# Optimization experiments

Measured on AMD Instinct MI355X. Metric: run time of the kernel, lower is better.

The kernel has to match this reference:

```python
import jax, jax.numpy as jnp
import numpy as np

LEAK = 0.01   # torch LeakyReLU default negative_slope
EPS = 1e-5    # torch BatchNorm2d default eps


def setup_inputs() -> dict:
    key = jax.random.key(0)
    ks = jax.random.split(key, 7)
    x = jax.random.normal(ks[0], (1, 64, 512, 512), jnp.float32)
    W = jax.random.normal(ks[1], (128, 64, 3, 3), jnp.float32) * 0.05
    gamma = jax.random.uniform(ks[2], (128,), jnp.float32, 0.5, 1.5)
    beta = jax.random.normal(ks[3], (128,), jnp.float32) * 0.1
    mean = jax.random.normal(ks[4], (128,), jnp.float32) * 0.1
    var = jax.random.uniform(ks[5], (128,), jnp.float32, 0.5, 1.5)
    # random.choices(rate=[0,1,1,...,1]) -> Bernoulli(0.9) mask over (1,C,H*W)
    mask = jax.random.bernoulli(ks[6], 0.9, (1, 128, 512, 512)).astype(jnp.int32)
    return dict(x=x, W=W, gamma=gamma, beta=beta, mean=mean, var=var, mask=mask)


def reference(x, W, gamma, beta, mean, var, mask):
    # 3x3 conv, stride 1, reflect padding 1, no bias
    xp = jnp.pad(x, ((0, 0), (0, 0), (1, 1), (1, 1)), mode='reflect')
    y = jax.lax.conv_general_dilated(
        xp, W, window_strides=(1, 1), padding='VALID',
        dimension_numbers=('NCHW', 'OIHW', 'NCHW'))
    # BatchNorm2d (inference mode: running stats)
    inv = jax.lax.rsqrt(var + EPS)
    scale = (gamma * inv)[None, :, None, None]
    shift = (beta - mean * gamma * inv)[None, :, None, None]
    y = y * scale + shift
    # Dropout2d(0.3) is identity in eval; LeakyReLU
    y = jnp.where(y >= 0, y, LEAK * y)
    # host-generated Bernoulli(0.9) mask multiply (the reshape to (1,C,1,H*W)
    # and back is a no-op on the math)
    return y * mask.astype(y.dtype)
```

## Files before the change

kernel.cpp:

```cpp
#include <hip/hip_runtime.h>

typedef unsigned short u16;
typedef unsigned int u32;
typedef __bf16 bf16x8 __attribute__((ext_vector_type(8)));
typedef float floatx4 __attribute__((ext_vector_type(4)));

#define EPS   1e-5f
#define LEAK  0.01f

#define TILE_H 4
#define TILE_W 64
#define IN_H   6
#define IN_W   66
#define CPAD   72

#define XT_BYTES ((size_t)512 * 512 * 64 * 2)
#define WT_BYTES ((size_t)9 * 128 * 64 * 2)

__device__ __forceinline__ u16 f2bf(float f) {
    union { float f; u32 i; } v; v.f = f;
    u32 i = v.i;
    return (u16)((i + 0x7fffu + ((i >> 16) & 1u)) >> 16);
}
__device__ __forceinline__ bf16x8 ld_frag(const u16* p) {
    uint4 d = *(const uint4*)p;
    return __builtin_bit_cast(bf16x8, d);
}

__global__ __launch_bounds__(256) void transpose_x(const float* __restrict__ x,
                                                   u16* __restrict__ xt)
{
    __shared__ u32 t[64][65];
    const int tid = threadIdx.x;
    const int s0  = blockIdx.x << 6;

    #pragma unroll
    for (int it = 0; it < 4; ++it) {
        int idx = it * 256 + tid;
        int ci = idx >> 4, wq = idx & 15;
        float4 d = *(const float4*)(x + (ci << 18) + s0 + (wq << 2));
        u32* row = &t[ci][wq << 2];
        row[0] = f2bf(d.x); row[1] = f2bf(d.y);
        row[2] = f2bf(d.z); row[3] = f2bf(d.w);
    }
    __syncthreads();
    #pragma unroll
    for (int it = 0; it < 2; ++it) {
        int idx = it * 256 + tid;
        int sl = idx >> 3, cb = idx & 7;
        uint4 o;
        o.x = t[cb * 8 + 0][sl] | (t[cb * 8 + 1][sl] << 16);
        o.y = t[cb * 8 + 2][sl] | (t[cb * 8 + 3][sl] << 16);
        o.z = t[cb * 8 + 4][sl] | (t[cb * 8 + 5][sl] << 16);
        o.w = t[cb * 8 + 6][sl] | (t[cb * 8 + 7][sl] << 16);
        *(uint4*)(xt + ((s0 + sl) << 6) + (cb << 3)) = o;
    }
}

__global__ __launch_bounds__(256) void transpose_w(const float* __restrict__ w,
                                                   u16* __restrict__ wt)
{
    int idx = blockIdx.x * 256 + threadIdx.x;
    int r   = idx >> 13;
    int rem = idx & 8191;
    wt[idx] = f2bf(w[rem * 9 + r]);
}

__global__ __launch_bounds__(256) void conv_mfma(
    const u16* __restrict__ xt,   const u16* __restrict__ wt,
    const float* __restrict__ gamma, const float* __restrict__ beta,
    const float* __restrict__ mean,  const float* __restrict__ var,
    const int* __restrict__ mask, float* __restrict__ out)
{
    __shared__ float s_scale[128];
    __shared__ float s_shift[128];
    __shared__ __attribute__((aligned(16))) u16 s_tile[IN_H * IN_W * CPAD];

    const int tid = threadIdx.x;
    const int bid = blockIdx.x;
    const int oh0 = (bid >> 3) << 2;
    const int ow0 = (bid & 7) << 6;

    if (tid < 128) {
        float sc = gamma[tid] * rsqrtf(var[tid] + EPS);
        s_scale[tid] = sc;
        s_shift[tid] = beta[tid] - mean[tid] * sc;
    }

    #pragma unroll
    for (int it = 0; it < 13; ++it) {
        int idx = it * 256 + tid;
        if (idx < IN_H * IN_W * 8) {
            int pos = idx >> 3, cb = idx & 7;
            int ihl = pos / IN_W;
            int iwl = pos - ihl * IN_W;
            int sh = oh0 - 1 + ihl; sh = sh < 0 ? -sh : (sh > 511 ? 1022 - sh : sh);
            int sw = ow0 - 1 + iwl; sw = sw < 0 ? -sw : (sw > 511 ? 1022 - sw : sw);
            uint4 d = *(const uint4*)(xt + (((sh << 9) + sw) << 6) + (cb << 3));
            *(uint4*)(s_tile + (ihl * IN_W + iwl) * CPAD + (cb << 3)) = d;
        }
    }
    __syncthreads();

    const int wave = tid >> 6;
    const int lane = tid & 63;
    const int quad = lane >> 4;
    const int l16  = lane & 15;
    const int mi   = wave >> 1;
    const int ni   = wave & 1;

    floatx4 acc[4][8];
    #pragma unroll
    for (int i = 0; i < 4; ++i)
        #pragma unroll
        for (int j = 0; j < 8; ++j)
            acc[i][j] = (floatx4){0.f, 0.f, 0.f, 0.f};

    int bbase[8];
    #pragma unroll
    for (int ns = 0; ns < 8; ++ns) {
        int n = ni * 128 + ns * 16 + l16;
        bbase[ns] = ((n >> 6) * IN_W + (n & 63)) * CPAD + quad * 8;
    }
    const u16* wbase = wt + (mi << 12) + (l16 << 6) + quad * 8;

    bf16x8 af_next[4];
    #pragma unroll
    for (int cs = 0; cs < 4; ++cs)
        af_next[cs] = ld_frag(wbase + (cs << 10));

    #pragma unroll 1
    for (int kc = 0; kc < 18; ++kc) {
        const int r    = kc >> 1;
        const int kh   = r / 3;
        const int kw   = r - kh * 3;
        const int cib  = (kc & 1) << 5;
        const int boff = (kh * IN_W + kw) * CPAD + cib;

        bf16x8 af[4];
        #pragma unroll
        for (int cs = 0; cs < 4; ++cs) af[cs] = af_next[cs];

        if (kc < 17) {
            const int kc1  = kc + 1;
            const int r1   = kc1 >> 1;
            const int cib1 = (kc1 & 1) << 5;
            #pragma unroll
            for (int cs = 0; cs < 4; ++cs)
                af_next[cs] = ld_frag(wbase + r1 * 8192 + (cs << 10) + cib1);
        }

        bf16x8 bfr[8];
        #pragma unroll
        for (int ns = 0; ns < 8; ++ns)
            bfr[ns] = ld_frag(s_tile + bbase[ns] + boff);

        #pragma unroll
        for (int cs = 0; cs < 4; ++cs)
            #pragma unroll
            for (int ns = 0; ns < 8; ++ns)
                acc[cs][ns] = __builtin_amdgcn_mfma_f32_16x16x32_bf16(
                    af[cs], bfr[ns], acc[cs][ns], 0, 0, 0);
    }

    int nbase[8];
    #pragma unroll
    for (int ns = 0; ns < 8; ++ns) {
        int n = ni * 128 + ns * 16 + l16;
        nbase[ns] = ((oh0 + (n >> 6)) << 9) + ow0 + (n & 63);
    }
    #pragma unroll
    for (int cs = 0; cs < 4; ++cs) {
        const int co0 = mi * 64 + cs * 16 + quad * 4;
        #pragma unroll
        for (int reg = 0; reg < 4; ++reg) {
            const int co = co0 + reg;
            const float sc = s_scale[co], sh = s_shift[co];
            const int cbase = co << 18;
            #pragma unroll
            for (int ns = 0; ns < 8; ++ns) {
                int idx = cbase + nbase[ns];
                float y = acc[cs][ns][reg] * sc + sh;
                y = (y >= 0.f) ? y : LEAK * y;
                y = mask[idx] ? y : 0.f;
                __builtin_nontemporal_store(y, &out[idx]);
            }
        }
    }
}

extern "C" void kernel_launch(void* const* d_in, const int* in_sizes, int n_in,
                              void* d_out, int out_size, void* d_ws, size_t ws_size,
                              hipStream_t stream)
{
    (void)in_sizes; (void)n_in; (void)out_size; (void)ws_size;
    const float* x     = (const float*)d_in[0];
    const float* W     = (const float*)d_in[1];
    const float* gamma = (const float*)d_in[2];
    const float* beta  = (const float*)d_in[3];
    const float* mean  = (const float*)d_in[4];
    const float* var   = (const float*)d_in[5];
    const int*   mask  = (const int*)d_in[6];
    float* out = (float*)d_out;

    u16* xt = (u16*)d_ws;
    u16* wt = (u16*)((char*)d_ws + XT_BYTES);

    transpose_w<<<288, 256, 0, stream>>>(W, wt);
    transpose_x<<<4096, 256, 0, stream>>>(x, xt);
    conv_mfma<<<1024, 256, 0, stream>>>(xt, wt, gamma, beta, mean, var, mask, out);
}
```

Baseline: 360.2 us.

## Fuse input transpose into conv kernel and shrink tile for occupancy

Drops the separate x-to-bf16 NHWC transpose kernel and its workspace round-trip. The conv kernel now reads fp32 NCHW input directly and converts to bf16 while staging into LDS. The output tile is halved to 4x32, giving 2048 blocks with fewer accumulators and a launch-bounds occupancy hint of 3. Mask loads become nontemporal. In exchange, the global loads during staging are strided by channel and less coalesced, and the larger halo ratio adds redundant input reads.

```diff
diff --git a/kernel.cpp b/kernel.cpp
--- a/kernel.cpp
+++ b/kernel.cpp
@@ -8,14 +8,10 @@
 #define EPS   1e-5f
 #define LEAK  0.01f
 
-#define TILE_H 4
-#define TILE_W 64
 #define IN_H   6
-#define IN_W   66
+#define IN_W   34
+#define NPOS   (IN_H * IN_W)
 #define CPAD   72
-
-#define XT_BYTES ((size_t)512 * 512 * 64 * 2)
-#define WT_BYTES ((size_t)9 * 128 * 64 * 2)
 
 __device__ __forceinline__ u16 f2bf(float f) {
     union { float f; u32 i; } v; v.f = f;
@@ -27,36 +23,6 @@
     return __builtin_bit_cast(bf16x8, d);
 }
 
-__global__ __launch_bounds__(256) void transpose_x(const float* __restrict__ x,
-                                                   u16* __restrict__ xt)
-{
-    __shared__ u32 t[64][65];
-    const int tid = threadIdx.x;
-    const int s0  = blockIdx.x << 6;
-
-    #pragma unroll
-    for (int it = 0; it < 4; ++it) {
-        int idx = it * 256 + tid;
-        int ci = idx >> 4, wq = idx & 15;
-        float4 d = *(const float4*)(x + (ci << 18) + s0 + (wq << 2));
-        u32* row = &t[ci][wq << 2];
-        row[0] = f2bf(d.x); row[1] = f2bf(d.y);
-        row[2] = f2bf(d.z); row[3] = f2bf(d.w);
-    }
-    __syncthreads();
-    #pragma unroll
-    for (int it = 0; it < 2; ++it) {
-        int idx = it * 256 + tid;
-        int sl = idx >> 3, cb = idx & 7;
-        uint4 o;
-        o.x = t[cb * 8 + 0][sl] | (t[cb * 8 + 1][sl] << 16);
-        o.y = t[cb * 8 + 2][sl] | (t[cb * 8 + 3][sl] << 16);
-        o.z = t[cb * 8 + 4][sl] | (t[cb * 8 + 5][sl] << 16);
-        o.w = t[cb * 8 + 6][sl] | (t[cb * 8 + 7][sl] << 16);
-        *(uint4*)(xt + ((s0 + sl) << 6) + (cb << 3)) = o;
-    }
-}
-
 __global__ __launch_bounds__(256) void transpose_w(const float* __restrict__ w,
                                                    u16* __restrict__ wt)
 {
@@ -66,20 +32,20 @@
     wt[idx] = f2bf(w[rem * 9 + r]);
 }
 
-__global__ __launch_bounds__(256) void conv_mfma(
-    const u16* __restrict__ xt,   const u16* __restrict__ wt,
+__global__ __launch_bounds__(256, 3) void conv_mfma(
+    const float* __restrict__ x,  const u16* __restrict__ wt,
     const float* __restrict__ gamma, const float* __restrict__ beta,
     const float* __restrict__ mean,  const float* __restrict__ var,
     const int* __restrict__ mask, float* __restrict__ out)
 {
     __shared__ float s_scale[128];
     __shared__ float s_shift[128];
-    __shared__ __attribute__((aligned(16))) u16 s_tile[IN_H * IN_W * CPAD];
+    __shared__ __attribute__((aligned(16))) u16 s_tile[NPOS * CPAD];
 
     const int tid = threadIdx.x;
     const int bid = blockIdx.x;
-    const int oh0 = (bid >> 3) << 2;
-    const int ow0 = (bid & 7) << 6;
+    const int oh0 = (bid >> 4) << 2;
+    const int ow0 = (bid & 15) << 5;
 
     if (tid < 128) {
         float sc = gamma[tid] * rsqrtf(var[tid] + EPS);
@@ -88,16 +54,25 @@
     }
 
     #pragma unroll
-    for (int it = 0; it < 13; ++it) {
-        int idx = it * 256 + tid;
-        if (idx < IN_H * IN_W * 8) {
-            int pos = idx >> 3, cb = idx & 7;
+    for (int it = 0; it < 7; ++it) {
+        int i = it * 256 + tid;
+        if (i < NPOS * 8) {
+            int cb  = i / NPOS;
+            int pos = i - cb * NPOS;
             int ihl = pos / IN_W;
             int iwl = pos - ihl * IN_W;
             int sh = oh0 - 1 + ihl; sh = sh < 0 ? -sh : (sh > 511 ? 1022 - sh : sh);
             int sw = ow0 - 1 + iwl; sw = sw < 0 ? -sw : (sw > 511 ? 1022 - sw : sw);
-            uint4 d = *(const uint4*)(xt + (((sh << 9) + sw) << 6) + (cb << 3));
-            *(uint4*)(s_tile + (ihl * IN_W + iwl) * CPAD + (cb << 3)) = d;
+            const float* src = x + (((size_t)cb << 21)) + (sh << 9) + sw;
+            float v0 = src[0 << 18], v1 = src[1 << 18], v2 = src[2 << 18],
+                  v3 = src[3 << 18], v4 = src[4 << 18], v5 = src[5 << 18],
+                  v6 = src[6 << 18], v7 = src[7 << 18];
+            uint4 p;
+            p.x = (u32)f2bf(v0) | ((u32)f2bf(v1) << 16);
+            p.y = (u32)f2bf(v2) | ((u32)f2bf(v3) << 16);
+            p.z = (u32)f2bf(v4) | ((u32)f2bf(v5) << 16);
+            p.w = (u32)f2bf(v6) | ((u32)f2bf(v7) << 16);
+            *(uint4*)(s_tile + pos * CPAD + (cb << 3)) = p;
         }
     }
     __syncthreads();
@@ -109,18 +84,18 @@
     const int mi   = wave >> 1;
     const int ni   = wave & 1;
 
-    floatx4 acc[4][8];
+    floatx4 acc[4][4];
     #pragma unroll
     for (int i = 0; i < 4; ++i)
         #pragma unroll
-        for (int j = 0; j < 8; ++j)
+        for (int j = 0; j < 4; ++j)
             acc[i][j] = (floatx4){0.f, 0.f, 0.f, 0.f};
 
-    int bbase[8];
+    int bbase[4];
     #pragma unroll
-    for (int ns = 0; ns < 8; ++ns) {
-        int n = ni * 128 + ns * 16 + l16;
-        bbase[ns] = ((n >> 6) * IN_W + (n & 63)) * CPAD + quad * 8;
+    for (int ns = 0; ns < 4; ++ns) {
+        int n = ni * 64 + ns * 16 + l16;
+        bbase[ns] = ((n >> 5) * IN_W + (n & 31)) * CPAD + quad * 8;
     }
     const u16* wbase = wt + (mi << 12) + (l16 << 6) + quad * 8;
 
@@ -150,24 +125,24 @@
                 af_next[cs] = ld_frag(wbase + r1 * 8192 + (cs << 10) + cib1);
         }
 
-        bf16x8 bfr[8];
+        bf16x8 bfr[4];
         #pragma unroll
-        for (int ns = 0; ns < 8; ++ns)
+        for (int ns = 0; ns < 4; ++ns)
             bfr[ns] = ld_frag(s_tile + bbase[ns] + boff);
 
         #pragma unroll
         for (int cs = 0; cs < 4; ++cs)
             #pragma unroll
-            for (int ns = 0; ns < 8; ++ns)
+            for (int ns = 0; ns < 4; ++ns)
                 acc[cs][ns] = __builtin_amdgcn_mfma_f32_16x16x32_bf16(
                     af[cs], bfr[ns], acc[cs][ns], 0, 0, 0);
     }
 
-    int nbase[8];
+    int nbase[4];
     #pragma unroll
-    for (int ns = 0; ns < 8; ++ns) {
-        int n = ni * 128 + ns * 16 + l16;
-        nbase[ns] = ((oh0 + (n >> 6)) << 9) + ow0 + (n & 63);
+    for (int ns = 0; ns < 4; ++ns) {
+        int n = ni * 64 + ns * 16 + l16;
+        nbase[ns] = ((oh0 + (n >> 5)) << 9) + ow0 + (n & 31);
     }
     #pragma unroll
     for (int cs = 0; cs < 4; ++cs) {
@@ -178,11 +153,12 @@
             const float sc = s_scale[co], sh = s_shift[co];
             const int cbase = co << 18;
             #pragma unroll
-            for (int ns = 0; ns < 8; ++ns) {
+            for (int ns = 0; ns < 4; ++ns) {
                 int idx = cbase + nbase[ns];
+                int m = __builtin_nontemporal_load(&mask[idx]);
                 float y = acc[cs][ns][reg] * sc + sh;
                 y = (y >= 0.f) ? y : LEAK * y;
-                y = mask[idx] ? y : 0.f;
+                y = m ? y : 0.f;
                 __builtin_nontemporal_store(y, &out[idx]);
             }
         }
@@ -203,10 +179,8 @@
     const int*   mask  = (const int*)d_in[6];
     float* out = (float*)d_out;
 
-    u16* xt = (u16*)d_ws;
-    u16* wt = (u16*)((char*)d_ws + XT_BYTES);
+    u16* wt = (u16*)d_ws;
 
     transpose_w<<<288, 256, 0, stream>>>(W, wt);
-    transpose_x<<<4096, 256, 0, stream>>>(x, xt);
-    conv_mfma<<<1024, 256, 0, stream>>>(xt, wt, gamma, beta, mean, var, mask, out);
+    conv_mfma<<<2048, 256, 0, stream>>>(x, wt, gamma, beta, mean, var, mask, out);
 }
```

After: 384.5 us. +6.8%, slower.

## Halve conv tile width and stage epilogue through LDS for vectorized stores

Applied to the files above, without the earlier changes.

The output tile shrinks from 4x64 to 4x32 pixels, so the grid doubles to 2048 blocks, per-wave accumulators halve and launch bounds request 4 blocks per SM for higher occupancy. The epilogue now writes MFMA accumulators into a shared-memory buffer that reuses the input tile space, then reads them back so each thread does 16-byte mask loads and 16-byte output stores. This replaces scattered scalar accesses. In exchange it adds extra syncs, LDS round trips, and more halo reloading, since the input tile is now 6x34 per 128 output pixels.

```diff
diff --git a/kernel.cpp b/kernel.cpp
--- a/kernel.cpp
+++ b/kernel.cpp
@@ -4,18 +4,18 @@
 typedef unsigned int u32;
 typedef __bf16 bf16x8 __attribute__((ext_vector_type(8)));
 typedef float floatx4 __attribute__((ext_vector_type(4)));
+typedef int   intx4   __attribute__((ext_vector_type(4)));
 
 #define EPS   1e-5f
 #define LEAK  0.01f
 
-#define TILE_H 4
-#define TILE_W 64
 #define IN_H   6
-#define IN_W   66
+#define IN_W   34
+#define NPOS   (IN_H * IN_W)
 #define CPAD   72
+#define CROW   132
 
 #define XT_BYTES ((size_t)512 * 512 * 64 * 2)
-#define WT_BYTES ((size_t)9 * 128 * 64 * 2)
 
 __device__ __forceinline__ u16 f2bf(float f) {
     union { float f; u32 i; } v; v.f = f;
@@ -66,7 +66,7 @@
     wt[idx] = f2bf(w[rem * 9 + r]);
 }
 
-__global__ __launch_bounds__(256) void conv_mfma(
+__global__ __launch_bounds__(256, 4) void conv_mfma(
     const u16* __restrict__ xt,   const u16* __restrict__ wt,
     const float* __restrict__ gamma, const float* __restrict__ beta,
     const float* __restrict__ mean,  const float* __restrict__ var,
@@ -74,12 +74,14 @@
 {
     __shared__ float s_scale[128];
     __shared__ float s_shift[128];
-    __shared__ __attribute__((aligned(16))) u16 s_tile[IN_H * IN_W * CPAD];
+    __shared__ __attribute__((aligned(16))) char smem[64 * CROW * 4];
+    u16*   s_tile = (u16*)smem;
+    float* cbuf   = (float*)smem;
 
     const int tid = threadIdx.x;
     const int bid = blockIdx.x;
-    const int oh0 = (bid >> 3) << 2;
-    const int ow0 = (bid & 7) << 6;
+    const int oh0 = (bid >> 4) << 2;
+    const int ow0 = (bid & 15) << 5;
 
     if (tid < 128) {
         float sc = gamma[tid] * rsqrtf(var[tid] + EPS);
@@ -88,16 +90,16 @@
     }
 
     #pragma unroll
-    for (int it = 0; it < 13; ++it) {
+    for (int it = 0; it < 7; ++it) {
         int idx = it * 256 + tid;
-        if (idx < IN_H * IN_W * 8) {
+        if (idx < NPOS * 8) {
             int pos = idx >> 3, cb = idx & 7;
             int ihl = pos / IN_W;
             int iwl = pos - ihl * IN_W;
             int sh = oh0 - 1 + ihl; sh = sh < 0 ? -sh : (sh > 511 ? 1022 - sh : sh);
             int sw = ow0 - 1 + iwl; sw = sw < 0 ? -sw : (sw > 511 ? 1022 - sw : sw);
             uint4 d = *(const uint4*)(xt + (((sh << 9) + sw) << 6) + (cb << 3));
-            *(uint4*)(s_tile + (ihl * IN_W + iwl) * CPAD + (cb << 3)) = d;
+            *(uint4*)(s_tile + pos * CPAD + (cb << 3)) = d;
         }
     }
     __syncthreads();
@@ -109,18 +111,18 @@
     const int mi   = wave >> 1;
     const int ni   = wave & 1;
 
-    floatx4 acc[4][8];
+    floatx4 acc[4][4];
     #pragma unroll
     for (int i = 0; i < 4; ++i)
         #pragma unroll
-        for (int j = 0; j < 8; ++j)
+        for (int j = 0; j < 4; ++j)
             acc[i][j] = (floatx4){0.f, 0.f, 0.f, 0.f};
 
-    int bbase[8];
-    #pragma unroll
-    for (int ns = 0; ns < 8; ++ns) {
-        int n = ni * 128 + ns * 16 + l16;
-        bbase[ns] = ((n >> 6) * IN_W + (n & 63)) * CPAD + quad * 8;
+    int bbase[4];
+    #pragma unroll
+    for (int ns = 0; ns < 4; ++ns) {
+        int n = ni * 64 + ns * 16 + l16;
+        bbase[ns] = ((n >> 5) * IN_W + (n & 31)) * CPAD + quad * 8;
     }
     const u16* wbase = wt + (mi << 12) + (l16 << 6) + quad * 8;
 
@@ -150,42 +152,55 @@
                 af_next[cs] = ld_frag(wbase + r1 * 8192 + (cs << 10) + cib1);
         }
 
-        bf16x8 bfr[8];
-        #pragma unroll
-        for (int ns = 0; ns < 8; ++ns)
+        bf16x8 bfr[4];
+        #pragma unroll
+        for (int ns = 0; ns < 4; ++ns)
             bfr[ns] = ld_frag(s_tile + bbase[ns] + boff);
 
         #pragma unroll
         for (int cs = 0; cs < 4; ++cs)
             #pragma unroll
-            for (int ns = 0; ns < 8; ++ns)
+            for (int ns = 0; ns < 4; ++ns)
                 acc[cs][ns] = __builtin_amdgcn_mfma_f32_16x16x32_bf16(
                     af[cs], bfr[ns], acc[cs][ns], 0, 0, 0);
     }
 
-    int nbase[8];
-    #pragma unroll
-    for (int ns = 0; ns < 8; ++ns) {
-        int n = ni * 128 + ns * 16 + l16;
-        nbase[ns] = ((oh0 + (n >> 6)) << 9) + ow0 + (n & 63);
-    }
-    #pragma unroll
-    for (int cs = 0; cs < 4; ++cs) {
-        const int co0 = mi * 64 + cs * 16 + quad * 4;
-        #pragma unroll
-        for (int reg = 0; reg < 4; ++reg) {
-            const int co = co0 + reg;
+    __syncthreads();
+
+    #pragma unroll
+    for (int c = 0; c < 2; ++c) {
+        #pragma unroll
+        for (int j = 0; j < 2; ++j) {
+            const int cs  = c * 2 + j;
+            const int row = mi * 32 + j * 16 + quad * 4;
+            #pragma unroll
+            for (int ns = 0; ns < 4; ++ns) {
+                const int n = ni * 64 + ns * 16 + l16;
+                float* p = cbuf + row * CROW + n;
+                #pragma unroll
+                for (int reg = 0; reg < 4; ++reg)
+                    p[reg * CROW] = acc[cs][ns][reg];
+            }
+        }
+        __syncthreads();
+        #pragma unroll
+        for (int k = 0; k < 8; ++k) {
+            const int idx = k * 256 + tid;
+            const int row = idx >> 5;
+            const int v   = idx & 31;
+            floatx4 y4 = *(const floatx4*)(cbuf + row * CROW + (v << 2));
+            const int co = ((row >> 5) << 6) + (c << 5) + (row & 31);
             const float sc = s_scale[co], sh = s_shift[co];
-            const int cbase = co << 18;
-            #pragma unroll
-            for (int ns = 0; ns < 8; ++ns) {
-                int idx = cbase + nbase[ns];
-                float y = acc[cs][ns][reg] * sc + sh;
-                y = (y >= 0.f) ? y : LEAK * y;
-                y = mask[idx] ? y : 0.f;
-                __builtin_nontemporal_store(y, &out[idx]);
-            }
-        }
+            const int gidx = (co << 18) + ((oh0 + (v >> 3)) << 9) + ow0 + ((v & 7) << 2);
+            intx4 m = __builtin_nontemporal_load((const intx4*)(mask + gidx));
+            floatx4 o;
+            float t0 = y4.x * sc + sh; o.x = m.x ? fmaxf(t0, t0 * LEAK) : 0.f;
+            float t1 = y4.y * sc + sh; o.y = m.y ? fmaxf(t1, t1 * LEAK) : 0.f;
+            float t2 = y4.z * sc + sh; o.z = m.z ? fmaxf(t2, t2 * LEAK) : 0.f;
+            float t3 = y4.w * sc + sh; o.w = m.w ? fmaxf(t3, t3 * LEAK) : 0.f;
+            __builtin_nontemporal_store(o, (floatx4*)(out + gidx));
+        }
+        if (c == 0) __syncthreads();
     }
 }
 
@@ -208,5 +223,5 @@
 
     transpose_w<<<288, 256, 0, stream>>>(W, wt);
     transpose_x<<<4096, 256, 0, stream>>>(x, xt);
-    conv_mfma<<<1024, 256, 0, stream>>>(xt, wt, gamma, beta, mean, var, mask, out);
-}
+    conv_mfma<<<2048, 256, 0, stream>>>(xt, wt, gamma, beta, mean, var, mask, out);
+}
```

Result: faster. 349.0 us (-3.1%).
